# Kernel tuning notes

Measured on AMD Instinct MI355X. Metric: run time of the kernel, lower is better.

## Reference

```python
import jax, jax.numpy as jnp
import numpy as np
from jax import lax

D_MODEL = 1024
EXPAND = 2
D_INNER = EXPAND * D_MODEL  # 2048
D_STATE = 16
D_CONV = 4
DT_RANK = -(-D_INNER // 16)  # ceil(d_inner/16) = 128
BATCH, SEQLEN = 2, 1024
LN_EPS = 1e-5


def setup_inputs() -> dict:
    key = jax.random.key(0)
    ks = jax.random.split(key, 8)
    s = lambda n: 1.0 / np.sqrt(n)
    x = jax.random.normal(ks[0], (BATCH, SEQLEN, D_MODEL), jnp.float32)
    ln_gamma = jnp.ones((D_MODEL,), jnp.float32)
    ln_beta = jnp.zeros((D_MODEL,), jnp.float32)
    in_proj_w = jax.random.normal(ks[1], (D_MODEL, 2 * D_INNER), jnp.float32) * s(D_MODEL)
    conv_w = jax.random.normal(ks[2], (D_INNER, D_CONV), jnp.float32) * s(D_CONV)
    conv_b = jnp.zeros((D_INNER,), jnp.float32)
    x_proj_w = jax.random.normal(ks[3], (D_INNER, DT_RANK + 2 * D_STATE), jnp.float32) * s(D_INNER)
    dt_proj_w = jax.random.uniform(ks[4], (DT_RANK, D_INNER), jnp.float32,
                                   -DT_RANK ** -0.5, DT_RANK ** -0.5)
    # dt bias init: inverse-softplus of dt ~ LogUniform(1e-3, 1e-1)
    dt = jnp.exp(jax.random.uniform(ks[5], (D_INNER,), jnp.float32)
                 * (np.log(0.1) - np.log(0.001)) + np.log(0.001))
    dt = jnp.clip(dt, 1e-4)
    dt_proj_b = dt + jnp.log(-jnp.expm1(-dt))
    A_log = jnp.log(jnp.tile(jnp.arange(1, D_STATE + 1, dtype=jnp.float32)[None, :],
                             (D_INNER, 1)))  # (D_INNER, D_STATE)
    D_param = jnp.ones((D_INNER,), jnp.float32)
    out_proj_w = jax.random.normal(ks[6], (D_INNER, D_MODEL), jnp.float32) * s(D_INNER)
    return {"x": x, "ln_gamma": ln_gamma, "ln_beta": ln_beta, "in_proj_w": in_proj_w,
            "conv_w": conv_w, "conv_b": conv_b, "x_proj_w": x_proj_w,
            "dt_proj_w": dt_proj_w, "dt_proj_b": dt_proj_b, "A_log": A_log,
            "D_param": D_param, "out_proj_w": out_proj_w}


def _layernorm(x, gamma, beta):
    mu = jnp.mean(x, -1, keepdims=True)
    var = jnp.mean(jnp.square(x - mu), -1, keepdims=True)
    return (x - mu) * lax.rsqrt(var + LN_EPS) * gamma + beta


def reference(x, ln_gamma, ln_beta, in_proj_w, conv_w, conv_b, x_proj_w,
              dt_proj_w, dt_proj_b, A_log, D_param, out_proj_w):
    B, L, _ = x.shape
    residual = x
    h = _layernorm(x, ln_gamma, ln_beta)
    xz = h @ in_proj_w                               # (B, L, 2*Di)
    xb, z = jnp.split(xz, 2, axis=-1)                # each (B, L, Di)

    # Depthwise causal conv1d (left pad d_conv-1, truncate to L)
    xp = jnp.pad(xb, ((0, 0), (D_CONV - 1, 0), (0, 0)))
    xc = sum(xp[:, k:k + L, :] * conv_w[:, k] for k in range(D_CONV)) + conv_b
    xb = jax.nn.silu(xc)                             # (B, L, Di)

    # Selective SSM
    xpj = xb @ x_proj_w                              # (B, L, dt_rank + 2N)
    dt_r = xpj[..., :DT_RANK]
    B_mat = xpj[..., DT_RANK:DT_RANK + D_STATE]      # (B, L, N)
    C_mat = xpj[..., DT_RANK + D_STATE:]             # (B, L, N)
    delta = jax.nn.softplus(dt_r @ dt_proj_w + dt_proj_b)  # (B, L, Di)
    A = -jnp.exp(A_log)                              # (Di, N)
    dA = jnp.exp(delta[..., None] * A)               # (B, L, Di, N)
    dBx = delta[..., None] * B_mat[:, :, None, :] * xb[..., None]  # (B, L, Di, N)

    def step(hcar, inp):
        dA_t, dBx_t, C_t = inp                       # (B,Di,N),(B,Di,N),(B,N)
        hcar = dA_t * hcar + dBx_t
        y_t = jnp.einsum('bdn,bn->bd', hcar, C_t)
        return hcar, y_t

    h0 = jnp.zeros((B, D_INNER, D_STATE), xb.dtype)
    _, ys = lax.scan(step, h0, (dA.transpose(1, 0, 2, 3),
                                dBx.transpose(1, 0, 2, 3),
                                C_mat.transpose(1, 0, 2)))
    y = ys.transpose(1, 0, 2) + xb * D_param         # (B, L, Di)

    y = y * jax.nn.silu(z)
    return y @ out_proj_w + residual
```

## Files before the change

### kernel.cpp

```cpp
#include <hip/hip_runtime.h>
#include <hip/hip_bf16.h>

#define D_MODEL 1024
#define D_INNER 2048
#define NPROJ   4096
#define D_STATE 16
#define DT_RANK 128
#define XPJ_N   160
#define SEQLEN  1024
#define BATCH   2
#define NTOK    2048
#define CHUNK   16
#define NCHUNK  (SEQLEN / CHUNK)
#define LOG2_NCHUNK 6
#define SPLITK  8
#define OP_SPLITK 4

typedef short short8 __attribute__((ext_vector_type(8)));
typedef unsigned short ushort8v __attribute__((ext_vector_type(8)));
typedef float f32x4 __attribute__((ext_vector_type(4)));

__device__ __forceinline__ float sigmoidf_(float x) { return 1.f / (1.f + __expf(-x)); }
__device__ __forceinline__ ushort f2bf_bits(float f) {
    __hip_bfloat16 h = __float2bfloat16(f);
    return *(ushort*)&h;
}
__device__ __forceinline__ float bf2f(ushort u) {
    union { unsigned int i; float f; } v;
    v.i = ((unsigned int)u) << 16;
    return v.f;
}
#define LOG2E 1.44269504088896f

__global__ __launch_bounds__(256) void ln_kernel(const float* __restrict__ x,
                                                 const float* __restrict__ g,
                                                 const float* __restrict__ be,
                                                 ushort* __restrict__ hb)
{
    int row = blockIdx.x;
    const float4* xr = (const float4*)(x + (long)row * D_MODEL);
    float4 v = xr[threadIdx.x];
    float s1 = v.x + v.y + v.z + v.w;
    float s2 = v.x*v.x + v.y*v.y + v.z*v.z + v.w*v.w;
    for (int off = 32; off >= 1; off >>= 1) {
        s1 += __shfl_down(s1, off);
        s2 += __shfl_down(s2, off);
    }
    __shared__ float red[8];
    int wid = threadIdx.x >> 6;
    if ((threadIdx.x & 63) == 0) { red[wid] = s1; red[4 + wid] = s2; }
    __syncthreads();
    float mu  = (red[0] + red[1] + red[2] + red[3]) * (1.f / D_MODEL);
    float ex2 = (red[4] + red[5] + red[6] + red[7]) * (1.f / D_MODEL);
    float inv = rsqrtf(ex2 - mu * mu + 1e-5f);
    float4 g4 = ((const float4*)g)[threadIdx.x];
    float4 b4 = ((const float4*)be)[threadIdx.x];
    ushort4 o;
    o.x = f2bf_bits((v.x - mu) * inv * g4.x + b4.x);
    o.y = f2bf_bits((v.y - mu) * inv * g4.y + b4.y);
    o.z = f2bf_bits((v.z - mu) * inv * g4.z + b4.z);
    o.w = f2bf_bits((v.w - mu) * inv * g4.w + b4.w);
    *(ushort4*)(hb + (long)row * D_MODEL + threadIdx.x * 4) = o;
}

__device__ __forceinline__ void transpose_tile(const float* __restrict__ in,
                                               ushort* __restrict__ out,
                                               int R, int C, int cx, int ry)
{
    __shared__ float tile[64][65];
    int c0 = cx * 64, r0 = ry * 64;
    #pragma unroll
    for (int i = 0; i < 16; ++i) {
        int idx = threadIdx.x + i * 256;
        int r = idx >> 6, c = idx & 63;
        tile[r][c] = (r0 + r < R && c0 + c < C) ? in[(long)(r0 + r) * C + (c0 + c)] : 0.f;
    }
    __syncthreads();
    #pragma unroll
    for (int i = 0; i < 16; ++i) {
        int idx = threadIdx.x + i * 256;
        int cc = idx >> 6, rr = idx & 63;
        if (c0 + cc < C && r0 + rr < R)
            out[(long)(c0 + cc) * R + (r0 + rr)] = f2bf_bits(tile[rr][cc]);
    }
}

__global__ __launch_bounds__(256) void transpose_all_kernel(const float* __restrict__ w2,
                                                            ushort* __restrict__ W2T,
                                                            const float* __restrict__ w7,
                                                            ushort* __restrict__ W7T,
                                                            const float* __restrict__ xp,
                                                            ushort* __restrict__ XPT,
                                                            const float* __restrict__ dt,
                                                            ushort* __restrict__ DTT)
{
    int idx = blockIdx.x;
    if (idx < 1024) {
        transpose_tile(w2, W2T, D_MODEL, NPROJ, idx & 63, idx >> 6);
    } else if (idx < 1536) {
        int rel = idx - 1024;
        transpose_tile(w7, W7T, D_INNER, D_MODEL, rel & 15, rel >> 4);
    } else if (idx < 1632) {
        int rel = idx - 1536;
        transpose_tile(xp, XPT, D_INNER, XPJ_N, rel % 3, rel / 3);
    } else {
        int rel = idx - 1632;
        transpose_tile(dt, DTT, DT_RANK, D_INNER, rel & 31, rel >> 5);
    }
}

template <int EPI, int OBF>
__global__ __launch_bounds__(256) void gemm_mfma_kernel(const ushort* __restrict__ A,
                                                        const ushort* __restrict__ Bt,
                                                        const float* __restrict__ bias,
                                                        float* __restrict__ Cf,
                                                        ushort* __restrict__ Cb,
                                                        int M, int N, int K, int lda, int ldb)
{
    long zoff = (long)blockIdx.z;
    A  += zoff * K;
    Bt += zoff * K;
    if (OBF == 0) Cf += zoff * (long)M * N;
    else          Cb += zoff * (long)M * N;
    int lin = blockIdx.y * gridDim.x + blockIdx.x;
    int cpx = (gridDim.x * gridDim.y) >> 3;
    lin = (lin & 7) * cpx + (lin >> 3);
    int bx = lin % gridDim.x, by = lin / gridDim.x;
    __shared__ __align__(16) ushort Al[2][128 * 32];
    __shared__ __align__(16) ushort Bl[2][128 * 32];
    int tid = threadIdx.x;
    int lane = tid & 63;
    int w = tid >> 6, wr = w >> 1, wc = w & 1;
    int m0 = by * 128, n0 = bx * 128;
    f32x4 acc[4][4];
    #pragma unroll
    for (int m = 0; m < 4; ++m)
        #pragma unroll
        for (int n = 0; n < 4; ++n) acc[m][n] = (f32x4){0.f, 0.f, 0.f, 0.f};
    int l15 = lane & 15, kq = lane >> 4;

    auto stage = [&](int buf, int k0) {
        #pragma unroll
        for (int i = 0; i < 2; ++i) {
            int s = i * 256 + tid;
            int row = s >> 2, kg = s & 3;
            int kgl = kg ^ ((row >> 1) & 3);
            __builtin_amdgcn_global_load_lds(
                (const __attribute__((address_space(1))) void*)(A + (long)(m0 + row) * lda + k0 + kgl * 8),
                (__attribute__((address_space(3))) void*)(Al[buf] + s * 8), 16, 0, 0);
            __builtin_amdgcn_global_load_lds(
                (const __attribute__((address_space(1))) void*)(Bt + (long)(n0 + row) * ldb + k0 + kgl * 8),
                (__attribute__((address_space(3))) void*)(Bl[buf] + s * 8), 16, 0, 0);
        }
    };

    stage(0, 0);
    int cur = 0;
    for (int k0 = 0; k0 < K; k0 += 32) {
        if (k0 + 32 < K) {
            stage(cur ^ 1, k0 + 32);
            asm volatile("s_waitcnt vmcnt(4)" ::: "memory");
        } else {
            asm volatile("s_waitcnt vmcnt(0)" ::: "memory");
        }
        __builtin_amdgcn_s_barrier();
        asm volatile("" ::: "memory");
        short8 af[4], bf[4];
        #pragma unroll
        for (int m = 0; m < 4; ++m) {
            int row = wr * 64 + m * 16 + l15;
            af[m] = *(const short8*)&Al[cur][row * 32 + (kq ^ ((row >> 1) & 3)) * 8];
        }
        #pragma unroll
        for (int n = 0; n < 4; ++n) {
            int row = wc * 64 + n * 16 + l15;
            bf[n] = *(const short8*)&Bl[cur][row * 32 + (kq ^ ((row >> 1) & 3)) * 8];
        }
        #pragma unroll
        for (int m = 0; m < 4; ++m)
            #pragma unroll
            for (int n = 0; n < 4; ++n)
                acc[m][n] = __builtin_amdgcn_mfma_f32_16x16x32_bf16(af[m], bf[n], acc[m][n], 0, 0, 0);
        asm volatile("" ::: "memory");
        __builtin_amdgcn_s_barrier();
        asm volatile("" ::: "memory");
        cur ^= 1;
    }
    #pragma unroll
    for (int m = 0; m < 4; ++m) {
        #pragma unroll
        for (int n = 0; n < 4; ++n) {
            #pragma unroll
            for (int r = 0; r < 4; ++r) {
                int row = m0 + wr * 64 + m * 16 + kq * 4 + r;
                int col = n0 + wc * 64 + n * 16 + l15;
                float v = acc[m][n][r];
                if (EPI == 1) {
                    v += bias[col];
                    v = (v > 20.f) ? v : log1pf(__expf(v));
                }
                if (OBF) Cb[(long)row * N + col] = f2bf_bits(v);
                else     Cf[(long)row * N + col] = v;
            }
        }
    }
}

template <int EPI, int OBF>
__global__ __launch_bounds__(256) void gemm_mfma64_kernel(const ushort* __restrict__ A,
                                                          const ushort* __restrict__ Bt,
                                                          const float* __restrict__ bias,
                                                          float* __restrict__ Cf,
                                                          ushort* __restrict__ Cb,
                                                          int M, int N, int K)
{
    int lin = blockIdx.y * gridDim.x + blockIdx.x;
    int cpx = (gridDim.x * gridDim.y) >> 3;
    lin = (lin & 7) * cpx + (lin >> 3);
    int bx = lin % gridDim.x, by = lin / gridDim.x;
    __shared__ __align__(16) ushort Al[2][128 * 32];
    __shared__ __align__(16) ushort Bl[2][64 * 32];
    int tid = threadIdx.x;
    int lane = tid & 63;
    int w = tid >> 6, wr = w >> 1, wc = w & 1;
    int m0 = by * 128, n0 = bx * 64;
    f32x4 acc[4][2];
    #pragma unroll
    for (int m = 0; m < 4; ++m)
        #pragma unroll
        for (int n = 0; n < 2; ++n) acc[m][n] = (f32x4){0.f, 0.f, 0.f, 0.f};
    int l15 = lane & 15, kq = lane >> 4;

    auto stage = [&](int buf, int k0) {
        #pragma unroll
        for (int i = 0; i < 2; ++i) {
            int s = i * 256 + tid;
            int row = s >> 2, kg = s & 3;
            int kgl = kg ^ ((row >> 1) & 3);
            __builtin_amdgcn_global_load_lds(
                (const __attribute__((address_space(1))) void*)(A + (long)(m0 + row) * K + k0 + kgl * 8),
                (__attribute__((address_space(3))) void*)(Al[buf] + s * 8), 16, 0, 0);
        }
        {
            int s = tid;
            int row = s >> 2, kg = s & 3;
            int kgl = kg ^ ((row >> 1) & 3);
            __builtin_amdgcn_global_load_lds(
                (const __attribute__((address_space(1))) void*)(Bt + (long)(n0 + row) * K + k0 + kgl * 8),
                (__attribute__((address_space(3))) void*)(Bl[buf] + s * 8), 16, 0, 0);
        }
    };

    stage(0, 0);
    int cur = 0;
    for (int k0 = 0; k0 < K; k0 += 32) {
        if (k0 + 32 < K) {
            stage(cur ^ 1, k0 + 32);
            asm volatile("s_waitcnt vmcnt(3)" ::: "memory");
        } else {
            asm volatile("s_waitcnt vmcnt(0)" ::: "memory");
        }
        __builtin_amdgcn_s_barrier();
        asm volatile("" ::: "memory");
        short8 af[4], bf[2];
        #pragma unroll
        for (int m = 0; m < 4; ++m) {
            int row = wr * 64 + m * 16 + l15;
            af[m] = *(const short8*)&Al[cur][row * 32 + (kq ^ ((row >> 1) & 3)) * 8];
        }
        #pragma unroll
        for (int n = 0; n < 2; ++n) {
            int row = wc * 32 + n * 16 + l15;
            bf[n] = *(const short8*)&Bl[cur][row * 32 + (kq ^ ((row >> 1) & 3)) * 8];
        }
        #pragma unroll
        for (int m = 0; m < 4; ++m)
            #pragma unroll
            for (int n = 0; n < 2; ++n)
                acc[m][n] = __builtin_amdgcn_mfma_f32_16x16x32_bf16(af[m], bf[n], acc[m][n], 0, 0, 0);
        asm volatile("" ::: "memory");
        __builtin_amdgcn_s_barrier();
        asm volatile("" ::: "memory");
        cur ^= 1;
    }
    #pragma unroll
    for (int m = 0; m < 4; ++m) {
        #pragma unroll
        for (int n = 0; n < 2; ++n) {
            #pragma unroll
            for (int r = 0; r < 4; ++r) {
                int row = m0 + wr * 64 + m * 16 + kq * 4 + r;
                int col = n0 + wc * 32 + n * 16 + l15;
                float v = acc[m][n][r];
                if (EPI == 1) {
                    v += bias[col];
                    v = (v > 20.f) ? v : log1pf(__expf(v));
                }
                if (OBF) Cb[(long)row * N + col] = f2bf_bits(v);
                else     Cf[(long)row * N + col] = v;
            }
        }
    }
}

__global__ __launch_bounds__(256) void reduce_out_kernel(const ushort* __restrict__ Ppart,
                                                         const float* __restrict__ resid,
                                                         float* __restrict__ out)
{
    long i = (long)blockIdx.x * 256 + threadIdx.x;
    const long STRIDE = (long)NTOK * D_MODEL;
    float4 s;
    ushort4 p0 = ((const ushort4*)Ppart)[i];
    s.x = bf2f(p0.x); s.y = bf2f(p0.y); s.z = bf2f(p0.z); s.w = bf2f(p0.w);
    #pragma unroll
    for (int k = 1; k < OP_SPLITK; ++k) {
        ushort4 pk = ((const ushort4*)(Ppart + k * STRIDE))[i];
        s.x += bf2f(pk.x); s.y += bf2f(pk.y); s.z += bf2f(pk.z); s.w += bf2f(pk.w);
    }
    float4 r = ((const float4*)resid)[i];
    s.x += r.x; s.y += r.y; s.z += r.z; s.w += r.w;
    ((float4*)out)[i] = s;
}

__global__ __launch_bounds__(256) void gemm4_mfma_kernel(const ushort* __restrict__ A,
                                                         const ushort* __restrict__ Bt,
                                                         ushort* __restrict__ Ppart,
                                                         int M, int K)
{
    __shared__ __align__(16) ushort Al[64 * 32];
    __shared__ __align__(16) ushort Bl[160 * 32];
    int tid = threadIdx.x;
    int lane = tid & 63;
    int w = tid >> 6, wr = w >> 1, wc = w & 1;
    int sk = blockIdx.x;
    int m0 = blockIdx.y * 64;
    int kbase = sk * (K / SPLITK);
    f32x4 acc[2][5];
    #pragma unroll
    for (int m = 0; m < 2; ++m)
        #pragma unroll
        for (int n = 0; n < 5; ++n) acc[m][n] = (f32x4){0.f, 0.f, 0.f, 0.f};
    int l15 = lane & 15, kq = lane >> 4;

    for (int ks = 0; ks < K / SPLITK; ks += 32) {
        int k0 = kbase + ks;
        {
            int s = tid;
            int row = s >> 2, kg = s & 3;
            int kgl = kg ^ ((row >> 1) & 3);
            __builtin_amdgcn_global_load_lds(
                (const __attribute__((address_space(1))) void*)(A + (long)(m0 + row) * K + k0 + kgl * 8),
                (__attribute__((address_space(3))) void*)(Al + s * 8), 16, 0, 0);
        }
        #pragma unroll
        for (int i = 0; i < 3; ++i) {
            int s = i * 256 + tid;
            if (s < 640) {
                int row = s >> 2, kg = s & 3;
                int kgl = kg ^ ((row >> 1) & 3);
                __builtin_amdgcn_global_load_lds(
                    (const __attribute__((address_space(1))) void*)(Bt + (long)row * K + k0 + kgl * 8),
                    (__attribute__((address_space(3))) void*)(Bl + s * 8), 16, 0, 0);
            }
        }
        __syncthreads();
        short8 af[2], bf[5];
        #pragma unroll
        for (int m = 0; m < 2; ++m) {
            int row = wr * 32 + m * 16 + l15;
            af[m] = *(const short8*)&Al[row * 32 + (kq ^ ((row >> 1) & 3)) * 8];
        }
        #pragma unroll
        for (int n = 0; n < 5; ++n) {
            int row = wc * 80 + n * 16 + l15;
            bf[n] = *(const short8*)&Bl[row * 32 + (kq ^ ((row >> 1) & 3)) * 8];
        }
        #pragma unroll
        for (int m = 0; m < 2; ++m)
            #pragma unroll
            for (int n = 0; n < 5; ++n)
                acc[m][n] = __builtin_amdgcn_mfma_f32_16x16x32_bf16(af[m], bf[n], acc[m][n], 0, 0, 0);
        __syncthreads();
    }
    ushort* P = Ppart + (long)sk * M * XPJ_N;
    #pragma unroll
    for (int m = 0; m < 2; ++m) {
        #pragma unroll
        for (int n = 0; n < 5; ++n) {
            #pragma unroll
            for (int r = 0; r < 4; ++r) {
                int row = m0 + wr * 32 + m * 16 + kq * 4 + r;
                int col = wc * 80 + n * 16 + l15;
                P[(long)row * XPJ_N + col] = f2bf_bits(acc[m][n][r]);
            }
        }
    }
}

__global__ __launch_bounds__(256) void reduce_xpj_kernel(const ushort* __restrict__ Ppart,
                                                         float* __restrict__ xpj,
                                                         ushort* __restrict__ dtr)
{
    long i = (long)blockIdx.x * 256 + threadIdx.x;
    float s = 0.f;
    #pragma unroll
    for (int k = 0; k < SPLITK; ++k) s += bf2f(Ppart[k * (long)NTOK * XPJ_N + i]);
    xpj[i] = s;
    int col = (int)(i % XPJ_N);
    long row = i / XPJ_N;
    if (col < DT_RANK) dtr[row * DT_RANK + col] = f2bf_bits(s);
}

__global__ __launch_bounds__(256) void conv_silu_kernel(const ushort* __restrict__ xzb,
                                                        const float* __restrict__ cw,
                                                        const float* __restrict__ cb,
                                                        ushort* __restrict__ xbb)
{
    long i = (long)blockIdx.x * 256 + threadIdx.x;
    int d8 = (int)(i & (D_INNER / 8 - 1));
    long tok = i >> 8;
    int l = (int)(tok & (SEQLEN - 1));
    int d0 = d8 * 8;
    const ushort* base = xzb + tok * NPROJ + d0;
    ushort8v r3 = *(const ushort8v*)base;
    ushort8v r2 = {0,0,0,0,0,0,0,0}, r1 = r2, r0 = r2;
    if (l >= 1) r2 = *(const ushort8v*)(base - NPROJ);
    if (l >= 2) r1 = *(const ushort8v*)(base - 2 * NPROJ);
    if (l >= 3) r0 = *(const ushort8v*)(base - 3 * NPROJ);
    ushort8v o;
    #pragma unroll
    for (int j = 0; j < 8; ++j) {
        int d = d0 + j;
        float4 wv = *(const float4*)&cw[d * 4];
        float acc = cb[d]
                  + bf2f(r0[j]) * wv.x + bf2f(r1[j]) * wv.y
                  + bf2f(r2[j]) * wv.z + bf2f(r3[j]) * wv.w;
        o[j] = f2bf_bits(acc * sigmoidf_(acc));
    }
    *(ushort8v*)(xbb + tok * D_INNER + d0) = o;
}

__global__ __launch_bounds__(256) void scan_partial_kernel(const ushort* __restrict__ deltab,
                                                           const ushort* __restrict__ xbb,
                                                           const float* __restrict__ xpj,
                                                           const float* __restrict__ A_log,
                                                           float* __restrict__ Pout,
                                                           float* __restrict__ Hout)
{
    __shared__ float bc[CHUNK][32];
    int blk = blockIdx.x;
    int db = blk & 7;
    int c  = (blk >> 3) & (NCHUNK - 1);
    int b  = blk >> (3 + LOG2_NCHUNK);
    int d  = db * 256 + threadIdx.x;
    long tok0 = (long)b * SEQLEN + c * CHUNK;
    for (int i = threadIdx.x; i < CHUNK * 32; i += 256) {
        int t = i >> 5, cc = i & 31;
        bc[t][cc] = xpj[(tok0 + t) * XPJ_N + DT_RANK + cc];
    }
    float a[16], h[16];
    #pragma unroll
    for (int q = 0; q < 4; ++q) {
        float4 al = *(const float4*)&A_log[d * D_STATE + q * 4];
        a[q*4+0] = -__expf(al.x) * LOG2E;
        a[q*4+1] = -__expf(al.y) * LOG2E;
        a[q*4+2] = -__expf(al.z) * LOG2E;
        a[q*4+3] = -__expf(al.w) * LOG2E;
    }
    #pragma unroll
    for (int n = 0; n < 16; ++n) h[n] = 0.f;
    float cum = 0.f;
    const ushort* dp = deltab + tok0 * D_INNER + d;
    const ushort* xp = xbb + tok0 * D_INNER + d;
    __syncthreads();
    #pragma unroll
    for (int t = 0; t < CHUNK; ++t) {
        float dl = bf2f(dp[(long)t * D_INNER]);
        float x  = bf2f(xp[(long)t * D_INNER]);
        float ux = dl * x;
        cum += dl;
        #pragma unroll
        for (int q = 0; q < 4; ++q) {
            float4 Bv = *(const float4*)&bc[t][q * 4];
            h[q*4+0] = exp2f(dl * a[q*4+0]) * h[q*4+0] + ux * Bv.x;
            h[q*4+1] = exp2f(dl * a[q*4+1]) * h[q*4+1] + ux * Bv.y;
            h[q*4+2] = exp2f(dl * a[q*4+2]) * h[q*4+2] + ux * Bv.z;
            h[q*4+3] = exp2f(dl * a[q*4+3]) * h[q*4+3] + ux * Bv.w;
        }
    }
    long chbase = ((long)(b * NCHUNK + c) * D_INNER + d) * D_STATE;
    #pragma unroll
    for (int q = 0; q < 4; ++q) {
        float4 pv = {exp2f(a[q*4+0] * cum), exp2f(a[q*4+1] * cum),
                     exp2f(a[q*4+2] * cum), exp2f(a[q*4+3] * cum)};
        *(float4*)&Pout[chbase + q * 4] = pv;
        float4 hv = {h[q*4+0], h[q*4+1], h[q*4+2], h[q*4+3]};
        *(float4*)&Hout[chbase + q * 4] = hv;
    }
}

__global__ __launch_bounds__(256) void scan_chunkscan_kernel(const float* __restrict__ P,
                                                             const float* __restrict__ H,
                                                             ushort* __restrict__ hinit)
{
    long i = (long)blockIdx.x * 256 + threadIdx.x;
    int n = (int)(i & (D_STATE - 1));
    int d = (int)((i >> 4) & (D_INNER - 1));
    int b = (int)(i >> 15);
    const long cstride = (long)D_INNER * D_STATE;
    long base = ((long)b * NCHUNK) * cstride + (long)d * D_STATE + n;
    float h = 0.f;
    for (int g = 0; g < NCHUNK / 8; ++g) {
        float Pr[8], Hr[8];
        #pragma unroll
        for (int j = 0; j < 8; ++j) {
            long o = base + (long)(g * 8 + j) * cstride;
            Pr[j] = P[o];
            Hr[j] = H[o];
        }
        #pragma unroll
        for (int j = 0; j < 8; ++j) {
            long o = base + (long)(g * 8 + j) * cstride;
            hinit[o] = f2bf_bits(h);
            h = Pr[j] * h + Hr[j];
        }
    }
}

__global__ __launch_bounds__(256) void scan_final_kernel(const ushort* __restrict__ deltab,
                                                         const ushort* __restrict__ xbb,
                                                         const float* __restrict__ xpj,
                                                         const ushort* __restrict__ xzb,
                                                         const float* __restrict__ A_log,
                                                         const float* __restrict__ Dp,
                                                         const ushort* __restrict__ hinit,
                                                         ushort* __restrict__ yb)
{
    __shared__ float bc[CHUNK][32];
    int blk = blockIdx.x;
    int db = blk & 7;
    int c  = (blk >> 3) & (NCHUNK - 1);
    int b  = blk >> (3 + LOG2_NCHUNK);
    int d  = db * 256 + threadIdx.x;
    long tok0 = (long)b * SEQLEN + c * CHUNK;
    for (int i = threadIdx.x; i < CHUNK * 32; i += 256) {
        int t = i >> 5, cc = i & 31;
        bc[t][cc] = xpj[(tok0 + t) * XPJ_N + DT_RANK + cc];
    }
    float a[16], h[16];
    #pragma unroll
    for (int q = 0; q < 4; ++q) {
        float4 al = *(const float4*)&A_log[d * D_STATE + q * 4];
        a[q*4+0] = -__expf(al.x) * LOG2E;
        a[q*4+1] = -__expf(al.y) * LOG2E;
        a[q*4+2] = -__expf(al.z) * LOG2E;
        a[q*4+3] = -__expf(al.w) * LOG2E;
    }
    long chbase = ((long)(b * NCHUNK + c) * D_INNER + d) * D_STATE;
    #pragma unroll
    for (int q = 0; q < 4; ++q) {
        ushort4 hv = *(const ushort4*)&hinit[chbase + q * 4];
        h[q*4+0] = bf2f(hv.x); h[q*4+1] = bf2f(hv.y);
        h[q*4+2] = bf2f(hv.z); h[q*4+3] = bf2f(hv.w);
    }
    float dpar = Dp[d];
    const ushort* dp = deltab + tok0 * D_INNER + d;
    const ushort* xp = xbb + tok0 * D_INNER + d;
    const ushort* zp = xzb + tok0 * NPROJ + D_INNER + d;
    ushort* yp = yb + tok0 * D_INNER + d;
    __syncthreads();
    #pragma unroll
    for (int t = 0; t < CHUNK; ++t) {
        float dl = bf2f(dp[(long)t * D_INNER]);
        float x  = bf2f(xp[(long)t * D_INNER]);
        float z  = bf2f(zp[(long)t * NPROJ]);
        float ux = dl * x;
        float y = 0.f;
        #pragma unroll
        for (int q = 0; q < 4; ++q) {
            float4 Bv = *(const float4*)&bc[t][q * 4];
            float4 Cv = *(const float4*)&bc[t][16 + q * 4];
            h[q*4+0] = exp2f(dl * a[q*4+0]) * h[q*4+0] + ux * Bv.x;
            h[q*4+1] = exp2f(dl * a[q*4+1]) * h[q*4+1] + ux * Bv.y;
            h[q*4+2] = exp2f(dl * a[q*4+2]) * h[q*4+2] + ux * Bv.z;
            h[q*4+3] = exp2f(dl * a[q*4+3]) * h[q*4+3] + ux * Bv.w;
            y += h[q*4+0] * Cv.x + h[q*4+1] * Cv.y + h[q*4+2] * Cv.z + h[q*4+3] * Cv.w;
        }
        y += x * dpar;
        yp[(long)t * D_INNER] = f2bf_bits(y * (z * sigmoidf_(z)));
    }
}

extern "C" void kernel_launch(void* const* d_in, const int* in_sizes, int n_in,
                              void* d_out, int out_size, void* d_ws, size_t ws_size,
                              hipStream_t stream) {
    const float* x         = (const float*)d_in[0];
    const float* ln_gamma  = (const float*)d_in[1];
    const float* ln_beta   = (const float*)d_in[2];
    const float* in_proj_w = (const float*)d_in[3];
    const float* conv_w    = (const float*)d_in[4];
    const float* conv_b    = (const float*)d_in[5];
    const float* x_proj_w  = (const float*)d_in[6];
    const float* dt_proj_w = (const float*)d_in[7];
    const float* dt_proj_b = (const float*)d_in[8];
    const float* A_log     = (const float*)d_in[9];
    const float* D_param   = (const float*)d_in[10];
    const float* out_proj_w= (const float*)d_in[11];
    float* out = (float*)d_out;

    float* p = (float*)d_ws;
    ushort* hb      = (ushort*)p; p += 1048576;
    ushort* W2T     = (ushort*)p; p += 2097152;
    ushort* W7T     = (ushort*)p; p += 1048576;
    ushort* XPT     = (ushort*)p; p += 163840;
    ushort* DTT     = (ushort*)p; p += 131072;
    ushort* xz_bf16 = (ushort*)p; p += 4194304;
    ushort* xb_bf16 = (ushort*)p; p += 2097152;
    float*  xpj     = p;          p += 327680;
    ushort* dtr     = (ushort*)p; p += 131072;
    ushort* delta_bf16 = (ushort*)p; p += 2097152;
    ushort* Ppart   = (ushort*)p; p += 1310720;
    float*  Pbuf    = p;          p += 4194304;
    float*  Hbuf    = p;          p += 4194304;
    ushort* hinit   = (ushort*)p; p += 2097152;
    ushort* y_bf16  = (ushort*)p; p += 2097152;
    ushort* PpartO  = (ushort*)p; p += 4194304;

    transpose_all_kernel<<<1696, 256, 0, stream>>>(
        in_proj_w, W2T, out_proj_w, W7T, x_proj_w, XPT, dt_proj_w, DTT);

    ln_kernel<<<NTOK, 256, 0, stream>>>(x, ln_gamma, ln_beta, hb);

    gemm_mfma_kernel<0, 1><<<dim3(NPROJ / 128, NTOK / 128), 256, 0, stream>>>(
        hb, W2T, nullptr, nullptr, xz_bf16, NTOK, NPROJ, D_MODEL, D_MODEL, D_MODEL);

    conv_silu_kernel<<<(NTOK * D_INNER / 8) / 256, 256, 0, stream>>>(
        xz_bf16, conv_w, conv_b, xb_bf16);

    gemm4_mfma_kernel<<<dim3(SPLITK, NTOK / 64), 256, 0, stream>>>(
        xb_bf16, XPT, Ppart, NTOK, D_INNER);
    reduce_xpj_kernel<<<(NTOK * XPJ_N) / 256, 256, 0, stream>>>(Ppart, xpj, dtr);

    gemm_mfma64_kernel<1, 1><<<dim3(D_INNER / 64, NTOK / 128), 256, 0, stream>>>(
        dtr, DTT, dt_proj_b, nullptr, delta_bf16, NTOK, D_INNER, DT_RANK);

    scan_partial_kernel<<<BATCH * NCHUNK * 8, 256, 0, stream>>>(
        delta_bf16, xb_bf16, xpj, A_log, Pbuf, Hbuf);
    scan_chunkscan_kernel<<<(BATCH * D_INNER * D_STATE) / 256, 256, 0, stream>>>(
        Pbuf, Hbuf, hinit);
    scan_final_kernel<<<BATCH * NCHUNK * 8, 256, 0, stream>>>(
        delta_bf16, xb_bf16, xpj, xz_bf16, A_log, D_param, hinit, y_bf16);

    gemm_mfma_kernel<0, 1><<<dim3(D_MODEL / 128, NTOK / 128, OP_SPLITK), 256, 0, stream>>>(
        y_bf16, W7T, nullptr, nullptr, PpartO, NTOK, D_MODEL, D_INNER / OP_SPLITK,
        D_INNER, D_INNER);
    reduce_out_kernel<<<(NTOK * D_MODEL / 4) / 256, 256, 0, stream>>>(PpartO, x, out);
}
```

Before: 173.2 us.

## Merge layernorm into transpose launch, bf16 scan carries, MFMA priority hints

Folds the layernorm rows into the weight-transpose kernel as extra blocks, removing one launch. Stores the per-chunk decay products P and chunk states H as bf16 instead of fp32, halving traffic between the partial-scan and chunk-scan kernels at some cost in precision. Raises wave priority around the MFMA loops in both GEMM kernels. Also shrinks the B-matrix staging in scan_partial to load only the 16 B columns it uses, with a single load per thread.

```diff
diff --git a/kernel.cpp b/kernel.cpp
--- a/kernel.cpp
+++ b/kernel.cpp
@@ -32,12 +32,34 @@
 }
 #define LOG2E 1.44269504088896f
 
-__global__ __launch_bounds__(256) void ln_kernel(const float* __restrict__ x,
-                                                 const float* __restrict__ g,
-                                                 const float* __restrict__ be,
-                                                 ushort* __restrict__ hb)
-{
-    int row = blockIdx.x;
+__device__ __forceinline__ void transpose_tile(const float* __restrict__ in,
+                                               ushort* __restrict__ out,
+                                               int R, int C, int cx, int ry)
+{
+    __shared__ float tile[64][65];
+    int c0 = cx * 64, r0 = ry * 64;
+    #pragma unroll
+    for (int i = 0; i < 16; ++i) {
+        int idx = threadIdx.x + i * 256;
+        int r = idx >> 6, c = idx & 63;
+        tile[r][c] = (r0 + r < R && c0 + c < C) ? in[(long)(r0 + r) * C + (c0 + c)] : 0.f;
+    }
+    __syncthreads();
+    #pragma unroll
+    for (int i = 0; i < 16; ++i) {
+        int idx = threadIdx.x + i * 256;
+        int cc = idx >> 6, rr = idx & 63;
+        if (c0 + cc < C && r0 + rr < R)
+            out[(long)(c0 + cc) * R + (r0 + rr)] = f2bf_bits(tile[rr][cc]);
+    }
+}
+
+__device__ __forceinline__ void ln_row(const float* __restrict__ x,
+                                       const float* __restrict__ g,
+                                       const float* __restrict__ be,
+                                       ushort* __restrict__ hb, int row)
+{
+    __shared__ float red[8];
     const float4* xr = (const float4*)(x + (long)row * D_MODEL);
     float4 v = xr[threadIdx.x];
     float s1 = v.x + v.y + v.z + v.w;
@@ -46,7 +68,6 @@
         s1 += __shfl_down(s1, off);
         s2 += __shfl_down(s2, off);
     }
-    __shared__ float red[8];
     int wid = threadIdx.x >> 6;
     if ((threadIdx.x & 63) == 0) { red[wid] = s1; red[4 + wid] = s2; }
     __syncthreads();
@@ -63,36 +84,18 @@
     *(ushort4*)(hb + (long)row * D_MODEL + threadIdx.x * 4) = o;
 }
 
-__device__ __forceinline__ void transpose_tile(const float* __restrict__ in,
-                                               ushort* __restrict__ out,
-                                               int R, int C, int cx, int ry)
-{
-    __shared__ float tile[64][65];
-    int c0 = cx * 64, r0 = ry * 64;
-    #pragma unroll
-    for (int i = 0; i < 16; ++i) {
-        int idx = threadIdx.x + i * 256;
-        int r = idx >> 6, c = idx & 63;
-        tile[r][c] = (r0 + r < R && c0 + c < C) ? in[(long)(r0 + r) * C + (c0 + c)] : 0.f;
-    }
-    __syncthreads();
-    #pragma unroll
-    for (int i = 0; i < 16; ++i) {
-        int idx = threadIdx.x + i * 256;
-        int cc = idx >> 6, rr = idx & 63;
-        if (c0 + cc < C && r0 + rr < R)
-            out[(long)(c0 + cc) * R + (r0 + rr)] = f2bf_bits(tile[rr][cc]);
-    }
-}
-
-__global__ __launch_bounds__(256) void transpose_all_kernel(const float* __restrict__ w2,
-                                                            ushort* __restrict__ W2T,
-                                                            const float* __restrict__ w7,
-                                                            ushort* __restrict__ W7T,
-                                                            const float* __restrict__ xp,
-                                                            ushort* __restrict__ XPT,
-                                                            const float* __restrict__ dt,
-                                                            ushort* __restrict__ DTT)
+__global__ __launch_bounds__(256) void prep_kernel(const float* __restrict__ w2,
+                                                   ushort* __restrict__ W2T,
+                                                   const float* __restrict__ w7,
+                                                   ushort* __restrict__ W7T,
+                                                   const float* __restrict__ xp,
+                                                   ushort* __restrict__ XPT,
+                                                   const float* __restrict__ dt,
+                                                   ushort* __restrict__ DTT,
+                                                   const float* __restrict__ x,
+                                                   const float* __restrict__ g,
+                                                   const float* __restrict__ be,
+                                                   ushort* __restrict__ hb)
 {
     int idx = blockIdx.x;
     if (idx < 1024) {
@@ -103,9 +106,11 @@
     } else if (idx < 1632) {
         int rel = idx - 1536;
         transpose_tile(xp, XPT, D_INNER, XPJ_N, rel % 3, rel / 3);
-    } else {
+    } else if (idx < 1696) {
         int rel = idx - 1632;
         transpose_tile(dt, DTT, DT_RANK, D_INNER, rel & 31, rel >> 5);
+    } else {
+        ln_row(x, g, be, hb, idx - 1696);
     }
 }
 
@@ -176,11 +181,13 @@
             int row = wc * 64 + n * 16 + l15;
             bf[n] = *(const short8*)&Bl[cur][row * 32 + (kq ^ ((row >> 1) & 3)) * 8];
         }
+        __builtin_amdgcn_s_setprio(1);
         #pragma unroll
         for (int m = 0; m < 4; ++m)
             #pragma unroll
             for (int n = 0; n < 4; ++n)
                 acc[m][n] = __builtin_amdgcn_mfma_f32_16x16x32_bf16(af[m], bf[n], acc[m][n], 0, 0, 0);
+        __builtin_amdgcn_s_setprio(0);
         asm volatile("" ::: "memory");
         __builtin_amdgcn_s_barrier();
         asm volatile("" ::: "memory");
@@ -273,11 +280,13 @@
             int row = wc * 32 + n * 16 + l15;
             bf[n] = *(const short8*)&Bl[cur][row * 32 + (kq ^ ((row >> 1) & 3)) * 8];
         }
+        __builtin_amdgcn_s_setprio(1);
         #pragma unroll
         for (int m = 0; m < 4; ++m)
             #pragma unroll
             for (int n = 0; n < 2; ++n)
                 acc[m][n] = __builtin_amdgcn_mfma_f32_16x16x32_bf16(af[m], bf[n], acc[m][n], 0, 0, 0);
+        __builtin_amdgcn_s_setprio(0);
         asm volatile("" ::: "memory");
         __builtin_amdgcn_s_barrier();
         asm volatile("" ::: "memory");
@@ -444,18 +453,18 @@
                                                            const ushort* __restrict__ xbb,
                                                            const float* __restrict__ xpj,
                                                            const float* __restrict__ A_log,
-                                                           float* __restrict__ Pout,
-                                                           float* __restrict__ Hout)
-{
-    __shared__ float bc[CHUNK][32];
+                                                           ushort* __restrict__ Pout,
+                                                           ushort* __restrict__ Hout)
+{
+    __shared__ float bc[CHUNK][16];
     int blk = blockIdx.x;
     int db = blk & 7;
     int c  = (blk >> 3) & (NCHUNK - 1);
     int b  = blk >> (3 + LOG2_NCHUNK);
     int d  = db * 256 + threadIdx.x;
     long tok0 = (long)b * SEQLEN + c * CHUNK;
-    for (int i = threadIdx.x; i < CHUNK * 32; i += 256) {
-        int t = i >> 5, cc = i & 31;
+    {
+        int t = threadIdx.x >> 4, cc = threadIdx.x & 15;
         bc[t][cc] = xpj[(tok0 + t) * XPJ_N + DT_RANK + cc];
     }
     float a[16], h[16];
@@ -491,16 +500,21 @@
     long chbase = ((long)(b * NCHUNK + c) * D_INNER + d) * D_STATE;
     #pragma unroll
     for (int q = 0; q < 4; ++q) {
-        float4 pv = {exp2f(a[q*4+0] * cum), exp2f(a[q*4+1] * cum),
-                     exp2f(a[q*4+2] * cum), exp2f(a[q*4+3] * cum)};
-        *(float4*)&Pout[chbase + q * 4] = pv;
-        float4 hv = {h[q*4+0], h[q*4+1], h[q*4+2], h[q*4+3]};
-        *(float4*)&Hout[chbase + q * 4] = hv;
-    }
-}
-
-__global__ __launch_bounds__(256) void scan_chunkscan_kernel(const float* __restrict__ P,
-                                                             const float* __restrict__ H,
+        ushort4 pv;
+        pv.x = f2bf_bits(exp2f(a[q*4+0] * cum));
+        pv.y = f2bf_bits(exp2f(a[q*4+1] * cum));
+        pv.z = f2bf_bits(exp2f(a[q*4+2] * cum));
+        pv.w = f2bf_bits(exp2f(a[q*4+3] * cum));
+        *(ushort4*)&Pout[chbase + q * 4] = pv;
+        ushort4 hv;
+        hv.x = f2bf_bits(h[q*4+0]); hv.y = f2bf_bits(h[q*4+1]);
+        hv.z = f2bf_bits(h[q*4+2]); hv.w = f2bf_bits(h[q*4+3]);
+        *(ushort4*)&Hout[chbase + q * 4] = hv;
+    }
+}
+
+__global__ __launch_bounds__(256) void scan_chunkscan_kernel(const ushort* __restrict__ P,
+                                                             const ushort* __restrict__ H,
                                                              ushort* __restrict__ hinit)
 {
     long i = (long)blockIdx.x * 256 + threadIdx.x;
@@ -511,7 +525,7 @@
     long base = ((long)b * NCHUNK) * cstride + (long)d * D_STATE + n;
     float h = 0.f;
     for (int g = 0; g < NCHUNK / 8; ++g) {
-        float Pr[8], Hr[8];
+        ushort Pr[8], Hr[8];
         #pragma unroll
         for (int j = 0; j < 8; ++j) {
             long o = base + (long)(g * 8 + j) * cstride;
@@ -522,7 +536,7 @@
         for (int j = 0; j < 8; ++j) {
             long o = base + (long)(g * 8 + j) * cstride;
             hinit[o] = f2bf_bits(h);
-            h = Pr[j] * h + Hr[j];
+            h = bf2f(Pr[j]) * h + bf2f(Hr[j]);
         }
     }
 }
@@ -620,16 +634,15 @@
     ushort* dtr     = (ushort*)p; p += 131072;
     ushort* delta_bf16 = (ushort*)p; p += 2097152;
     ushort* Ppart   = (ushort*)p; p += 1310720;
-    float*  Pbuf    = p;          p += 4194304;
-    float*  Hbuf    = p;          p += 4194304;
+    ushort* Pbuf    = (ushort*)p; p += 2097152;
+    ushort* Hbuf    = (ushort*)p; p += 2097152;
     ushort* hinit   = (ushort*)p; p += 2097152;
     ushort* y_bf16  = (ushort*)p; p += 2097152;
     ushort* PpartO  = (ushort*)p; p += 4194304;
 
-    transpose_all_kernel<<<1696, 256, 0, stream>>>(
-        in_proj_w, W2T, out_proj_w, W7T, x_proj_w, XPT, dt_proj_w, DTT);
-
-    ln_kernel<<<NTOK, 256, 0, stream>>>(x, ln_gamma, ln_beta, hb);
+    prep_kernel<<<1696 + NTOK, 256, 0, stream>>>(
+        in_proj_w, W2T, out_proj_w, W7T, x_proj_w, XPT, dt_proj_w, DTT,
+        x, ln_gamma, ln_beta, hb);
 
     gemm_mfma_kernel<0, 1><<<dim3(NPROJ / 128, NTOK / 128), 256, 0, stream>>>(
         hb, W2T, nullptr, nullptr, xz_bf16, NTOK, NPROJ, D_MODEL, D_MODEL, D_MODEL);
```

Measured after the change: 166.3 us (median of 3 runs). 1.04x faster.
